# Kernel optimization log

Measured on AMD Instinct MI355X. Metric: run time of the kernel, lower is better.

## Reference

```python
import jax, jax.numpy as jnp
import numpy as np

QMAX = 127.0

def _quantize_int8(x, axis):
    """Symmetric dynamic int8 quantization along `axis`. Returns (int8 values, fp32 scale)."""
    amax = jnp.max(jnp.abs(x), axis=axis, keepdims=True)
    scale = jnp.maximum(amax, 1e-8) / QMAX
    q = jnp.clip(jnp.round(x / scale), -QMAX, QMAX).astype(jnp.int8)
    return q, scale


def setup_inputs() -> dict:
    key = jax.random.key(0)
    kx, kw, kb = jax.random.split(key, 3)
    tokens, d_in, d_out = 4096, 4096, 16384
    x = jax.random.normal(kx, (tokens, d_in), dtype=jnp.float32)
    weight = jax.random.normal(kw, (d_out, d_in), dtype=jnp.float32) * (1.0 / np.sqrt(d_in))
    bias = jax.random.normal(kb, (d_out,), dtype=jnp.float32)
    return {"x": x, "weight": weight, "bias": bias}


def reference(x, weight, bias):
    # Quantize activations per-row (over in_features), weights per-output-column.
    xq, sx = _quantize_int8(x, axis=-1)            # [T, in] int8, [T, 1] scale
    wq, sw = _quantize_int8(weight.T, axis=0)      # [in, out] int8, [1, out] scale
    acc = jnp.matmul(xq, wq, preferred_element_type=jnp.int32)  # [T, out] int32
    out = acc.astype(jnp.float32) * sx * sw + bias
    return out
```

## Files before the change

kernel.cpp:

```cpp
#include <hip/hip_runtime.h>
#include <stdint.h>

typedef int   i32x4  __attribute__((ext_vector_type(4)));
typedef int   i32x16 __attribute__((ext_vector_type(16)));
typedef float f32x4  __attribute__((ext_vector_type(4)));

#define AS1 __attribute__((address_space(1)))
#define AS3 __attribute__((address_space(3)))
#define G2L16(gp, lp) __builtin_amdgcn_global_load_lds((const AS1 void*)(gp), (AS3 void*)(lp), 16, 0, 0)

template<int COLS>
__global__ __launch_bounds__(256)
void quant_rows_k(const float* __restrict__ src, int8_t* __restrict__ q,
                  float* __restrict__ scale)
{
    constexpr int PER = COLS / 256;
    static_assert(PER == 16, "pack assumes 16 elems/thread");
    const int row = blockIdx.x;
    const int t   = threadIdx.x;
    const float* s = src + (size_t)row * COLS + (size_t)t * PER;

    float v[PER];
    #pragma unroll
    for (int i = 0; i < PER; i += 4) {
        f32x4 x4 = *reinterpret_cast<const f32x4*>(s + i);
        v[i+0] = x4[0]; v[i+1] = x4[1]; v[i+2] = x4[2]; v[i+3] = x4[3];
    }
    float amax = 0.0f;
    #pragma unroll
    for (int i = 0; i < PER; ++i) amax = fmaxf(amax, fabsf(v[i]));

    #pragma unroll
    for (int off = 32; off > 0; off >>= 1)
        amax = fmaxf(amax, __shfl_xor(amax, off, 64));

    __shared__ float red[4];
    if ((t & 63) == 0) red[t >> 6] = amax;
    __syncthreads();
    amax = fmaxf(fmaxf(red[0], red[1]), fmaxf(red[2], red[3]));

    const float sc = fmaxf(amax, 1e-8f) / 127.0f;
    if (t == 0) scale[row] = sc;

    union { i32x4 v4; int8_t b[16]; } pk;
    #pragma unroll
    for (int i = 0; i < PER; ++i) {
        float r = rintf(v[i] / sc);
        r = fminf(127.0f, fmaxf(-127.0f, r));
        pk.b[i] = (int8_t)r;
    }
    *reinterpret_cast<i32x4*>(q + (size_t)row * COLS + (size_t)t * PER) = pk.v4;
}

#define BM 256
#define BN 256
#define BKB 128

__device__ __forceinline__ i32x16 mfma32(i32x4 a, i32x4 b, i32x16 c) {
    return __builtin_amdgcn_mfma_i32_32x32x32_i8(a, b, c, 0, 0, 0);
}
__device__ __forceinline__ i32x4 ldsld(const int8_t* p) {
    return *reinterpret_cast<const i32x4*>(p);
}
#define FENCE asm volatile("" ::: "memory")
#define BAR   do { FENCE; __builtin_amdgcn_s_barrier(); FENCE; } while (0)
#define LGKM0 asm volatile("s_waitcnt lgkmcnt(0)" ::: "memory")
#define SCHB  __builtin_amdgcn_sched_barrier(0)

template<bool ST>
__device__ __forceinline__ void tile_fn(
    const int8_t* __restrict__ aP, const int8_t* __restrict__ bP,
    i32x16 (&acc)[4][2],
    const int8_t* __restrict__ gA, const int8_t* __restrict__ gB,
    int8_t* lAn, int8_t* lBn,
    size_t r128, int t16)
{
    i32x4 a00 = ldsld(aP + 0);
    i32x4 a01 = ldsld(aP + 1024);
    i32x4 a10 = ldsld(aP + 2048);
    i32x4 a11 = ldsld(aP + 3072);
    i32x4 b00 = ldsld(bP + 0);
    i32x4 b01 = ldsld(bP + 1024);
    i32x4 b10 = ldsld(bP + 2048);
    i32x4 b11 = ldsld(bP + 3072);
    if (ST) {
        G2L16(gB,        lBn + t16);
        G2L16(gB + r128, lBn + 8192 + t16);
    }
    BAR; LGKM0; SCHB;
    __builtin_amdgcn_s_setprio(1);
    acc[0][0] = mfma32(a00, b00, acc[0][0]);
    acc[1][0] = mfma32(a10, b00, acc[1][0]);
    acc[0][1] = mfma32(a00, b10, acc[0][1]);
    acc[1][1] = mfma32(a10, b10, acc[1][1]);
    acc[0][0] = mfma32(a01, b01, acc[0][0]);
    acc[1][0] = mfma32(a11, b01, acc[1][0]);
    acc[0][1] = mfma32(a01, b11, acc[0][1]);
    acc[1][1] = mfma32(a11, b11, acc[1][1]);
    __builtin_amdgcn_s_setprio(0);
    BAR;
    i32x4 a20 = ldsld(aP + 4096);
    i32x4 a21 = ldsld(aP + 5120);
    i32x4 a30 = ldsld(aP + 6144);
    i32x4 a31 = ldsld(aP + 7168);
    if (ST) {
        G2L16(gB + 64,        lBn + 16384 + t16);
        G2L16(gB + r128 + 64, lBn + 24576 + t16);
    }
    BAR; LGKM0; SCHB;
    __builtin_amdgcn_s_setprio(1);
    acc[2][0] = mfma32(a20, b00, acc[2][0]);
    acc[3][0] = mfma32(a30, b00, acc[3][0]);
    acc[2][1] = mfma32(a20, b10, acc[2][1]);
    acc[3][1] = mfma32(a30, b10, acc[3][1]);
    acc[2][0] = mfma32(a21, b01, acc[2][0]);
    acc[3][0] = mfma32(a31, b01, acc[3][0]);
    acc[2][1] = mfma32(a21, b11, acc[2][1]);
    acc[3][1] = mfma32(a31, b11, acc[3][1]);
    __builtin_amdgcn_s_setprio(0);
    if (ST) asm volatile("s_waitcnt vmcnt(4)" ::: "memory");
    else    asm volatile("s_waitcnt vmcnt(0)" ::: "memory");
    BAR;
    i32x4 c00 = ldsld(aP + 16384);
    i32x4 c01 = ldsld(aP + 17408);
    i32x4 c10 = ldsld(aP + 18432);
    i32x4 c11 = ldsld(aP + 19456);
    i32x4 d00 = ldsld(bP + 16384);
    i32x4 d01 = ldsld(bP + 17408);
    i32x4 d10 = ldsld(bP + 18432);
    i32x4 d11 = ldsld(bP + 19456);
    if (ST) {
        G2L16(gA,        lAn + t16);
        G2L16(gA + r128, lAn + 8192 + t16);
    }
    BAR; LGKM0; SCHB;
    __builtin_amdgcn_s_setprio(1);
    acc[0][0] = mfma32(c00, d00, acc[0][0]);
    acc[1][0] = mfma32(c10, d00, acc[1][0]);
    acc[0][1] = mfma32(c00, d10, acc[0][1]);
    acc[1][1] = mfma32(c10, d10, acc[1][1]);
    acc[0][0] = mfma32(c01, d01, acc[0][0]);
    acc[1][0] = mfma32(c11, d01, acc[1][0]);
    acc[0][1] = mfma32(c01, d11, acc[0][1]);
    acc[1][1] = mfma32(c11, d11, acc[1][1]);
    __builtin_amdgcn_s_setprio(0);
    BAR;
    i32x4 e00 = ldsld(aP + 20480);
    i32x4 e01 = ldsld(aP + 21504);
    i32x4 e10 = ldsld(aP + 22528);
    i32x4 e11 = ldsld(aP + 23552);
    if (ST) {
        G2L16(gA + 64,        lAn + 16384 + t16);
        G2L16(gA + r128 + 64, lAn + 24576 + t16);
    }
    BAR; LGKM0; SCHB;
    __builtin_amdgcn_s_setprio(1);
    acc[2][0] = mfma32(e00, d00, acc[2][0]);
    acc[3][0] = mfma32(e10, d00, acc[3][0]);
    acc[2][1] = mfma32(e00, d10, acc[2][1]);
    acc[3][1] = mfma32(e10, d10, acc[3][1]);
    acc[2][0] = mfma32(e01, d01, acc[2][0]);
    acc[3][0] = mfma32(e11, d01, acc[3][0]);
    acc[2][1] = mfma32(e01, d11, acc[2][1]);
    acc[3][1] = mfma32(e11, d11, acc[3][1]);
    __builtin_amdgcn_s_setprio(0);
    if (ST) asm volatile("s_waitcnt vmcnt(2)" ::: "memory");
    else    asm volatile("s_waitcnt vmcnt(0)" ::: "memory");
    BAR;
}

__global__ __launch_bounds__(512, 2)
void gemm_i8_k(const int8_t* __restrict__ A,
               const int8_t* __restrict__ B,
               const float*  __restrict__ sx,
               const float*  __restrict__ sw,
               const float*  __restrict__ bias,
               float* __restrict__ C,
               int M, int N, int K)
{
    __shared__ int8_t lA[2][32768];
    __shared__ int8_t lB[2][32768];

    const int t    = threadIdx.x;
    const int lane = t & 63;
    const int wid  = t >> 6;
    const int wm   = wid >> 2;
    const int wn   = wid & 3;

    const int nwg = (int)gridDim.x;
    const int bid = (int)blockIdx.x;
    const int swz = ((nwg & 7) == 0) ? ((bid & 7) * (nwg >> 3) + (bid >> 3)) : bid;
    const int nbn = N / BN;
    const int bm  = swz / nbn;
    const int bn  = swz % nbn;

    const int8_t* aP0 = &lA[0][wm * 8192 + lane * 16];
    const int8_t* aP1 = &lA[1][wm * 8192 + lane * 16];
    const int8_t* bP0 = &lB[0][(wn >> 1) * 8192 + (wn & 1) * 4096 + lane * 16];
    const int8_t* bP1 = &lB[1][(wn >> 1) * 8192 + (wn & 1) * 4096 + lane * 16];

    const int rS = ((t >> 7) * 32) + (t & 31);
    const int kS = ((t >> 6) & 1) * 32 + ((t >> 5) & 1) * 16;
    const int t16 = t * 16;
    const int8_t* pA = A + (size_t)(bm * BM + rS) * K + kS;
    const int8_t* pB = B + (size_t)(bn * BN + rS) * K + kS;
    const size_t r128 = (size_t)128 * K;

    G2L16(pB,              &lB[0][0]     + t16);
    G2L16(pB + r128,       &lB[0][8192]  + t16);
    G2L16(pB + 64,         &lB[0][16384] + t16);
    G2L16(pB + r128 + 64,  &lB[0][24576] + t16);
    G2L16(pA,              &lA[0][0]     + t16);
    G2L16(pA + r128,       &lA[0][8192]  + t16);
    G2L16(pA + 64,         &lA[0][16384] + t16);
    G2L16(pA + r128 + 64,  &lA[0][24576] + t16);
    asm volatile("s_waitcnt vmcnt(2)" ::: "memory");
    BAR;

    i32x16 acc[4][2] = {};

    const int NT = K / BKB;
    for (int tt = 0; tt + 2 < NT; tt += 2) {
        const size_t ko1 = (size_t)(tt + 1) * BKB;
        tile_fn<true>(aP0, bP0, acc, pA + ko1, pB + ko1, &lA[1][0], &lB[1][0], r128, t16);
        const size_t ko2 = (size_t)(tt + 2) * BKB;
        tile_fn<true>(aP1, bP1, acc, pA + ko2, pB + ko2, &lA[0][0], &lB[0][0], r128, t16);
    }
    {
        const size_t ko1 = (size_t)(NT - 1) * BKB;
        tile_fn<true >(aP0, bP0, acc, pA + ko1, pB + ko1, &lA[1][0], &lB[1][0], r128, t16);
        tile_fn<false>(aP1, bP1, acc, pA, pB, &lA[0][0], &lB[0][0], r128, t16);
    }

    const int hi   = lane >> 5;
    const int col0 = bn * BN + wn * 64 + (lane & 31);
    #pragma unroll
    for (int ni = 0; ni < 2; ++ni) {
        const int c = col0 + ni * 32;
        const float swc = sw[c];
        const float bc  = bias[c];
        #pragma unroll
        for (int mi = 0; mi < 4; ++mi) {
            const int rb = bm * BM + wm * 128 + mi * 32 + 4 * hi;
            #pragma unroll
            for (int r = 0; r < 16; ++r) {
                const int row = rb + (r & 3) + 8 * (r >> 2);
                C[(size_t)row * N + c] = (float)acc[mi][ni][r] * sx[row] * swc + bc;
            }
        }
    }
}

extern "C" void kernel_launch(void* const* d_in, const int* in_sizes, int n_in,
                              void* d_out, int out_size, void* d_ws, size_t ws_size,
                              hipStream_t stream) {
    const float* x    = (const float*)d_in[0];
    const float* w    = (const float*)d_in[1];
    const float* bias = (const float*)d_in[2];
    float* out = (float*)d_out;

    const int dout   = in_sizes[2];
    const int din    = in_sizes[1] / dout;
    const int tokens = in_sizes[0] / din;

    char* ws = (char*)d_ws;
    float*  sx = (float*)ws;
    float*  sw = (float*)(ws + 16384);
    int8_t* xq = (int8_t*)(ws + 16384 + 65536);
    int8_t* wq = xq + (size_t)tokens * din;

    quant_rows_k<4096><<<tokens, 256, 0, stream>>>(x, xq, sx);
    quant_rows_k<4096><<<dout,   256, 0, stream>>>(w, wq, sw);

    const int grid = (tokens / BM) * (dout / BN);
    gemm_i8_k<<<grid, 512, 0, stream>>>(xq, wq, sx, sw, bias, out, tokens, dout, din);
}
```

Before: 509.2 us.

## Switch GEMM LDS tiles to row-major XOR-swizzled layout with contiguous row loads

Changes the shared-memory layout of the A and B tiles from a k-split blocked arrangement to row-major 128-byte rows with an XOR swizzle on the 16-byte chunk index. Each thread now fetches one full row's chunk from global memory (8 threads per row), so global reads become more contiguous, and the swizzle is meant to avoid LDS bank conflicts on the MFMA operand reads. The per-tile schedule is reordered so all four k-chunks for each A half are consumed together, with B fragments kept in registers longer. This raises register pressure and adds XOR offset arithmetic, and the interleaving of async stores against LDS reads has to stay race-free.

```diff
diff --git a/kernel.cpp b/kernel.cpp
--- a/kernel.cpp
+++ b/kernel.cpp
@@ -69,100 +69,101 @@
 
 template<bool ST>
 __device__ __forceinline__ void tile_fn(
-    const int8_t* __restrict__ aP, const int8_t* __restrict__ bP,
+    const int8_t* __restrict__ aB, const int8_t* __restrict__ bB,
+    int kc0, int kc1, int kc2, int kc3,
     i32x16 (&acc)[4][2],
     const int8_t* __restrict__ gA, const int8_t* __restrict__ gB,
     int8_t* lAn, int8_t* lBn,
-    size_t r128, int t16)
+    size_t r64, size_t r128, int t16)
 {
-    i32x4 a00 = ldsld(aP + 0);
-    i32x4 a01 = ldsld(aP + 1024);
-    i32x4 a10 = ldsld(aP + 2048);
-    i32x4 a11 = ldsld(aP + 3072);
-    i32x4 b00 = ldsld(bP + 0);
-    i32x4 b01 = ldsld(bP + 1024);
-    i32x4 b10 = ldsld(bP + 2048);
-    i32x4 b11 = ldsld(bP + 3072);
-    if (ST) {
-        G2L16(gB,        lBn + t16);
-        G2L16(gB + r128, lBn + 8192 + t16);
-    }
-    BAR; LGKM0; SCHB;
-    __builtin_amdgcn_s_setprio(1);
-    acc[0][0] = mfma32(a00, b00, acc[0][0]);
-    acc[1][0] = mfma32(a10, b00, acc[1][0]);
-    acc[0][1] = mfma32(a00, b10, acc[0][1]);
-    acc[1][1] = mfma32(a10, b10, acc[1][1]);
-    acc[0][0] = mfma32(a01, b01, acc[0][0]);
-    acc[1][0] = mfma32(a11, b01, acc[1][0]);
-    acc[0][1] = mfma32(a01, b11, acc[0][1]);
-    acc[1][1] = mfma32(a11, b11, acc[1][1]);
-    __builtin_amdgcn_s_setprio(0);
-    BAR;
-    i32x4 a20 = ldsld(aP + 4096);
-    i32x4 a21 = ldsld(aP + 5120);
-    i32x4 a30 = ldsld(aP + 6144);
-    i32x4 a31 = ldsld(aP + 7168);
-    if (ST) {
-        G2L16(gB + 64,        lBn + 16384 + t16);
-        G2L16(gB + r128 + 64, lBn + 24576 + t16);
-    }
-    BAR; LGKM0; SCHB;
-    __builtin_amdgcn_s_setprio(1);
-    acc[2][0] = mfma32(a20, b00, acc[2][0]);
-    acc[3][0] = mfma32(a30, b00, acc[3][0]);
-    acc[2][1] = mfma32(a20, b10, acc[2][1]);
-    acc[3][1] = mfma32(a30, b10, acc[3][1]);
-    acc[2][0] = mfma32(a21, b01, acc[2][0]);
-    acc[3][0] = mfma32(a31, b01, acc[3][0]);
-    acc[2][1] = mfma32(a21, b11, acc[2][1]);
-    acc[3][1] = mfma32(a31, b11, acc[3][1]);
+    if (ST) {
+        G2L16(gB,       lBn + t16);
+        G2L16(gB + r64, lBn + 8192 + t16);
+    }
+    i32x4 A00 = ldsld(aB + 0*4096 + kc0);
+    i32x4 A01 = ldsld(aB + 0*4096 + kc1);
+    i32x4 A10 = ldsld(aB + 1*4096 + kc0);
+    i32x4 A11 = ldsld(aB + 1*4096 + kc1);
+    i32x4 B00 = ldsld(bB + 0*4096 + kc0);
+    i32x4 B01 = ldsld(bB + 0*4096 + kc1);
+    i32x4 B10 = ldsld(bB + 1*4096 + kc0);
+    i32x4 B11 = ldsld(bB + 1*4096 + kc1);
+    BAR; LGKM0; SCHB;
+    __builtin_amdgcn_s_setprio(1);
+    acc[0][0] = mfma32(A00, B00, acc[0][0]);
+    acc[1][0] = mfma32(A10, B00, acc[1][0]);
+    acc[0][1] = mfma32(A00, B10, acc[0][1]);
+    acc[1][1] = mfma32(A10, B10, acc[1][1]);
+    acc[0][0] = mfma32(A01, B01, acc[0][0]);
+    acc[1][0] = mfma32(A11, B01, acc[1][0]);
+    acc[0][1] = mfma32(A01, B11, acc[0][1]);
+    acc[1][1] = mfma32(A11, B11, acc[1][1]);
+    __builtin_amdgcn_s_setprio(0);
+    BAR;
+    if (ST) {
+        G2L16(gB + 2*r64, lBn + 16384 + t16);
+        G2L16(gB + 3*r64, lBn + 24576 + t16);
+    }
+    i32x4 A02 = ldsld(aB + 0*4096 + kc2);
+    i32x4 A03 = ldsld(aB + 0*4096 + kc3);
+    i32x4 A12 = ldsld(aB + 1*4096 + kc2);
+    i32x4 A13 = ldsld(aB + 1*4096 + kc3);
+    i32x4 B02 = ldsld(bB + 0*4096 + kc2);
+    i32x4 B03 = ldsld(bB + 0*4096 + kc3);
+    i32x4 B12 = ldsld(bB + 1*4096 + kc2);
+    i32x4 B13 = ldsld(bB + 1*4096 + kc3);
+    BAR; LGKM0; SCHB;
+    __builtin_amdgcn_s_setprio(1);
+    acc[0][0] = mfma32(A02, B02, acc[0][0]);
+    acc[1][0] = mfma32(A12, B02, acc[1][0]);
+    acc[0][1] = mfma32(A02, B12, acc[0][1]);
+    acc[1][1] = mfma32(A12, B12, acc[1][1]);
+    acc[0][0] = mfma32(A03, B03, acc[0][0]);
+    acc[1][0] = mfma32(A13, B03, acc[1][0]);
+    acc[0][1] = mfma32(A03, B13, acc[0][1]);
+    acc[1][1] = mfma32(A13, B13, acc[1][1]);
     __builtin_amdgcn_s_setprio(0);
     if (ST) asm volatile("s_waitcnt vmcnt(4)" ::: "memory");
     else    asm volatile("s_waitcnt vmcnt(0)" ::: "memory");
     BAR;
-    i32x4 c00 = ldsld(aP + 16384);
-    i32x4 c01 = ldsld(aP + 17408);
-    i32x4 c10 = ldsld(aP + 18432);
-    i32x4 c11 = ldsld(aP + 19456);
-    i32x4 d00 = ldsld(bP + 16384);
-    i32x4 d01 = ldsld(bP + 17408);
-    i32x4 d10 = ldsld(bP + 18432);
-    i32x4 d11 = ldsld(bP + 19456);
     if (ST) {
         G2L16(gA,        lAn + t16);
-        G2L16(gA + r128, lAn + 8192 + t16);
-    }
-    BAR; LGKM0; SCHB;
-    __builtin_amdgcn_s_setprio(1);
-    acc[0][0] = mfma32(c00, d00, acc[0][0]);
-    acc[1][0] = mfma32(c10, d00, acc[1][0]);
-    acc[0][1] = mfma32(c00, d10, acc[0][1]);
-    acc[1][1] = mfma32(c10, d10, acc[1][1]);
-    acc[0][0] = mfma32(c01, d01, acc[0][0]);
-    acc[1][0] = mfma32(c11, d01, acc[1][0]);
-    acc[0][1] = mfma32(c01, d11, acc[0][1]);
-    acc[1][1] = mfma32(c11, d11, acc[1][1]);
-    __builtin_amdgcn_s_setprio(0);
-    BAR;
-    i32x4 e00 = ldsld(aP + 20480);
-    i32x4 e01 = ldsld(aP + 21504);
-    i32x4 e10 = ldsld(aP + 22528);
-    i32x4 e11 = ldsld(aP + 23552);
-    if (ST) {
-        G2L16(gA + 64,        lAn + 16384 + t16);
-        G2L16(gA + r128 + 64, lAn + 24576 + t16);
-    }
-    BAR; LGKM0; SCHB;
-    __builtin_amdgcn_s_setprio(1);
-    acc[2][0] = mfma32(e00, d00, acc[2][0]);
-    acc[3][0] = mfma32(e10, d00, acc[3][0]);
-    acc[2][1] = mfma32(e00, d10, acc[2][1]);
-    acc[3][1] = mfma32(e10, d10, acc[3][1]);
-    acc[2][0] = mfma32(e01, d01, acc[2][0]);
-    acc[3][0] = mfma32(e11, d01, acc[3][0]);
-    acc[2][1] = mfma32(e01, d11, acc[2][1]);
-    acc[3][1] = mfma32(e11, d11, acc[3][1]);
+        G2L16(gA + r128, lAn + 16384 + t16);
+    }
+    i32x4 A20 = ldsld(aB + 2*4096 + kc0);
+    i32x4 A21 = ldsld(aB + 2*4096 + kc1);
+    i32x4 A30 = ldsld(aB + 3*4096 + kc0);
+    i32x4 A31 = ldsld(aB + 3*4096 + kc1);
+    BAR; LGKM0; SCHB;
+    __builtin_amdgcn_s_setprio(1);
+    acc[2][0] = mfma32(A20, B00, acc[2][0]);
+    acc[3][0] = mfma32(A30, B00, acc[3][0]);
+    acc[2][1] = mfma32(A20, B10, acc[2][1]);
+    acc[3][1] = mfma32(A30, B10, acc[3][1]);
+    acc[2][0] = mfma32(A21, B01, acc[2][0]);
+    acc[3][0] = mfma32(A31, B01, acc[3][0]);
+    acc[2][1] = mfma32(A21, B11, acc[2][1]);
+    acc[3][1] = mfma32(A31, B11, acc[3][1]);
+    __builtin_amdgcn_s_setprio(0);
+    BAR;
+    if (ST) {
+        G2L16(gA + r64,        lAn + 8192  + t16);
+        G2L16(gA + r128 + r64, lAn + 24576 + t16);
+    }
+    i32x4 A22 = ldsld(aB + 2*4096 + kc2);
+    i32x4 A23 = ldsld(aB + 2*4096 + kc3);
+    i32x4 A32 = ldsld(aB + 3*4096 + kc2);
+    i32x4 A33 = ldsld(aB + 3*4096 + kc3);
+    BAR; LGKM0; SCHB;
+    __builtin_amdgcn_s_setprio(1);
+    acc[2][0] = mfma32(A22, B02, acc[2][0]);
+    acc[3][0] = mfma32(A32, B02, acc[3][0]);
+    acc[2][1] = mfma32(A22, B12, acc[2][1]);
+    acc[3][1] = mfma32(A32, B12, acc[3][1]);
+    acc[2][0] = mfma32(A23, B03, acc[2][0]);
+    acc[3][0] = mfma32(A33, B03, acc[3][0]);
+    acc[2][1] = mfma32(A23, B13, acc[2][1]);
+    acc[3][1] = mfma32(A33, B13, acc[3][1]);
     __builtin_amdgcn_s_setprio(0);
     if (ST) asm volatile("s_waitcnt vmcnt(2)" ::: "memory");
     else    asm volatile("s_waitcnt vmcnt(0)" ::: "memory");
@@ -178,8 +179,8 @@
                float* __restrict__ C,
                int M, int N, int K)
 {
-    __shared__ int8_t lA[2][32768];
-    __shared__ int8_t lB[2][32768];
+    __shared__ int8_t lA[2][BM * BKB];
+    __shared__ int8_t lB[2][BN * BKB];
 
     const int t    = threadIdx.x;
     const int lane = t & 63;
@@ -194,26 +195,36 @@
     const int bm  = swz / nbn;
     const int bn  = swz % nbn;
 
-    const int8_t* aP0 = &lA[0][wm * 8192 + lane * 16];
-    const int8_t* aP1 = &lA[1][wm * 8192 + lane * 16];
-    const int8_t* bP0 = &lB[0][(wn >> 1) * 8192 + (wn & 1) * 4096 + lane * 16];
-    const int8_t* bP1 = &lB[1][(wn >> 1) * 8192 + (wn & 1) * 4096 + lane * 16];
-
-    const int rS = ((t >> 7) * 32) + (t & 31);
-    const int kS = ((t >> 6) & 1) * 32 + ((t >> 5) & 1) * 16;
-    const int t16 = t * 16;
-    const int8_t* pA = A + (size_t)(bm * BM + rS) * K + kS;
-    const int8_t* pB = B + (size_t)(bn * BN + rS) * K + kS;
+    const int r31 = lane & 31;
+    const int hi  = lane >> 5;
+    const int sw8 = lane & 7;
+    const int kc0 = ((0 + hi) ^ sw8) << 4;
+    const int kc1 = ((2 + hi) ^ sw8) << 4;
+    const int kc2 = ((4 + hi) ^ sw8) << 4;
+    const int kc3 = ((6 + hi) ^ sw8) << 4;
+    const int aOff = (wm * 128 + r31) * BKB;
+    const int bOff = (wn * 64 + r31) * BKB;
+    const int8_t* aB0 = &lA[0][aOff];
+    const int8_t* aB1 = &lA[1][aOff];
+    const int8_t* bB0 = &lB[0][bOff];
+    const int8_t* bB1 = &lB[1][bOff];
+
+    const int srow = t >> 3;
+    const int skc  = ((t & 7) ^ (srow & 7)) * 16;
+    const int t16  = t * 16;
+    const int8_t* pA = A + (size_t)(bm * BM + srow) * K + skc;
+    const int8_t* pB = B + (size_t)(bn * BN + srow) * K + skc;
+    const size_t r64  = (size_t)64  * K;
     const size_t r128 = (size_t)128 * K;
 
     G2L16(pB,              &lB[0][0]     + t16);
-    G2L16(pB + r128,       &lB[0][8192]  + t16);
-    G2L16(pB + 64,         &lB[0][16384] + t16);
-    G2L16(pB + r128 + 64,  &lB[0][24576] + t16);
+    G2L16(pB + r64,        &lB[0][8192]  + t16);
+    G2L16(pB + 2*r64,      &lB[0][16384] + t16);
+    G2L16(pB + 3*r64,      &lB[0][24576] + t16);
     G2L16(pA,              &lA[0][0]     + t16);
-    G2L16(pA + r128,       &lA[0][8192]  + t16);
-    G2L16(pA + 64,         &lA[0][16384] + t16);
-    G2L16(pA + r128 + 64,  &lA[0][24576] + t16);
+    G2L16(pA + r128,       &lA[0][16384] + t16);
+    G2L16(pA + r64,        &lA[0][8192]  + t16);
+    G2L16(pA + r128 + r64, &lA[0][24576] + t16);
     asm volatile("s_waitcnt vmcnt(2)" ::: "memory");
     BAR;
 
@@ -222,18 +233,17 @@
     const int NT = K / BKB;
     for (int tt = 0; tt + 2 < NT; tt += 2) {
         const size_t ko1 = (size_t)(tt + 1) * BKB;
-        tile_fn<true>(aP0, bP0, acc, pA + ko1, pB + ko1, &lA[1][0], &lB[1][0], r128, t16);
+        tile_fn<true>(aB0, bB0, kc0, kc1, kc2, kc3, acc, pA + ko1, pB + ko1, &lA[1][0], &lB[1][0], r64, r128, t16);
         const size_t ko2 = (size_t)(tt + 2) * BKB;
-        tile_fn<true>(aP1, bP1, acc, pA + ko2, pB + ko2, &lA[0][0], &lB[0][0], r128, t16);
+        tile_fn<true>(aB1, bB1, kc0, kc1, kc2, kc3, acc, pA + ko2, pB + ko2, &lA[0][0], &lB[0][0], r64, r128, t16);
     }
     {
         const size_t ko1 = (size_t)(NT - 1) * BKB;
-        tile_fn<true >(aP0, bP0, acc, pA + ko1, pB + ko1, &lA[1][0], &lB[1][0], r128, t16);
-        tile_fn<false>(aP1, bP1, acc, pA, pB, &lA[0][0], &lB[0][0], r128, t16);
-    }
-
-    const int hi   = lane >> 5;
-    const int col0 = bn * BN + wn * 64 + (lane & 31);
+        tile_fn<true >(aB0, bB0, kc0, kc1, kc2, kc3, acc, pA + ko1, pB + ko1, &lA[1][0], &lB[1][0], r64, r128, t16);
+        tile_fn<false>(aB1, bB1, kc0, kc1, kc2, kc3, acc, pA, pB, &lA[0][0], &lB[0][0], r64, r128, t16);
+    }
+
+    const int col0 = bn * BN + wn * 64 + r31;
     #pragma unroll
     for (int ni = 0; ni < 2; ++ni) {
         const int c = col0 + ni * 32;
```

Result: faster. 485.0 us (-4.7%).
